# Optimization experiments

Hardware: AMD Instinct MI355X
Metric: run time of the kernel (lower is better)

## Reference

```python
import jax, jax.numpy as jnp
import numpy as np

B_SZ, T, H, N, L = 4, 512, 256, 64, 4
EPS = 1e-5

def _hippo(n):
    i = np.arange(n)[:, None]; j = np.arange(n)[None, :]
    A = np.where(i >= j, ((-1.0) ** (i - j)) * np.sqrt((2 * i + 1.0) * (2 * j + 1.0)), 0.0)
    # scale to be contractive so the 512-step dense recurrence stays finite
    A = A / (1.1 * np.linalg.norm(A, 2))
    return A.astype(np.float32)

def _xavier(key, shape):
    fan_in, fan_out = shape[1], shape[0]
    a = float(np.sqrt(6.0 / (fan_in + fan_out)))
    return jax.random.uniform(key, shape, jnp.float32, -a, a)

def setup_inputs() -> dict:
    key = jax.random.key(0)
    ks = jax.random.split(key, 8)
    x = jax.random.normal(ks[0], (B_SZ, T, H), jnp.float32)
    A = jnp.broadcast_to(jnp.asarray(_hippo(N)), (L, N, N))
    Bm = jnp.stack([_xavier(jax.random.fold_in(ks[1], l), (N, H)) for l in range(L)])
    Cm = jnp.stack([_xavier(jax.random.fold_in(ks[2], l), (H, N)) for l in range(L)])
    Dm = jnp.stack([_xavier(jax.random.fold_in(ks[3], l), (H, H)) for l in range(L)])
    Win = _xavier(ks[4], (H, H)); bin_ = jnp.zeros((H,), jnp.float32)
    Wout = _xavier(ks[5], (H, H)); bout = jnp.zeros((H,), jnp.float32)
    return {"x": x, "Win": Win, "bin_": bin_, "Wout": Wout, "bout": bout,
            "A": A, "Bm": Bm, "Cm": Cm, "Dm": Dm}

def _ln(x):
    m = jnp.mean(x, -1, keepdims=True)
    v = jnp.mean((x - m) ** 2, -1, keepdims=True)
    return (x - m) / jnp.sqrt(v + EPS)

def _ssm_layer(h, A, B, C, D):
    # h: (B,T,H); dense state (B,N,H)
    Cbar = C.mean(0)            # mean over output rows (matches C_state.mean(dim=2))
    BT = B.T                    # (H,N)
    DT = D.T                    # (H,H)
    def step(state, u):        # state (B,N,H), u (B,H)
        y = jnp.einsum('bnh,n->bh', state, Cbar) + u @ DT   # output uses pre-update state
        new_state = jnp.einsum('nm,bmh->bnh', A, state) + (u @ BT)[:, :, None]
        return new_state, y
    state0 = jnp.zeros((h.shape[0], A.shape[0], h.shape[2]), h.dtype)
    _, ys = jax.lax.scan(step, state0, jnp.swapaxes(h, 0, 1))  # scan over T
    y = jnp.swapaxes(ys, 0, 1)
    y = jax.nn.gelu(y, approximate=False) + h   # GELU -> (dropout=0) -> residual
    return _ln(y)

def reference(x, Win, bin_, Wout, bout, A, Bm, Cm, Dm):
    h = x @ Win.T + bin_
    for l in range(L):
        h = _ssm_layer(h, A[l], Bm[l], Cm[l], Dm[l])
    h = _ln(h)
    return h @ Wout.T + bout
```

## Files before the change

### kernel.cpp

```cpp
#include <hip/hip_runtime.h>

#define TSEQ 512
#define HDIM 256
#define NDIM 64
#define LC   48
#define YSTR 260
#define NWB  128

typedef __attribute__((ext_vector_type(4))) float  f32x4;
typedef __attribute__((ext_vector_type(8))) short  s16x8;
typedef __attribute__((ext_vector_type(4))) unsigned short u16x4;
typedef unsigned long long u64;
typedef unsigned short us;

#define MFMA16 __builtin_amdgcn_mfma_f32_16x16x32_bf16

__device__ __forceinline__ float wave_red(float v) {
#pragma unroll
    for (int m = 1; m < 64; m <<= 1) v += __shfl_xor(v, m, 64);
    return v;
}
__device__ __forceinline__ float lane_bcast(float v, int l) {
    return __int_as_float(__builtin_amdgcn_readlane(__float_as_int(v), l));
}
__device__ __forceinline__ us f2bf(float f) {
    unsigned u = __float_as_uint(f);
    u += 0x7fffu + ((u >> 16) & 1u);
    return (us)(u >> 16);
}
__device__ __forceinline__ float bf2f(us h) {
    return __uint_as_float(((unsigned)h) << 16);
}
__device__ __forceinline__ int swz(int row, int chunk) {
    return row * 512 + (((chunk) ^ (row & 7)) << 4);
}

__device__ __forceinline__ void st_mall(float* p, float v) {
    __hip_atomic_store(p, v, __ATOMIC_RELAXED, __HIP_MEMORY_SCOPE_AGENT);
}
__device__ __forceinline__ u64 ld_mall8(const u64* p) {
    return __hip_atomic_load(p, __ATOMIC_RELAXED, __HIP_MEMORY_SCOPE_AGENT);
}
__device__ __forceinline__ void flag_set(unsigned* f) {
    __hip_atomic_store(f, 1u, __ATOMIC_RELAXED, __HIP_MEMORY_SCOPE_AGENT);
}
__device__ __forceinline__ void flag_wait(const unsigned* f) {
    while (__hip_atomic_load(f, __ATOMIC_RELAXED, __HIP_MEMORY_SCOPE_AGENT) == 0u)
        __builtin_amdgcn_s_sleep(1);
}

__global__ void __launch_bounds__(256) k_prep(
    const float* __restrict__ Win, const float* __restrict__ Wout,
    const float* __restrict__ Bm, const float* __restrict__ Dm,
    const float* __restrict__ Cm, const float* __restrict__ A,
    us* __restrict__ Win_bf, us* __restrict__ Wout_bf,
    us* __restrict__ Bm_bf, us* __restrict__ Dm_bf,
    float* __restrict__ cbar_g, float* __restrict__ wA8,
    unsigned* __restrict__ flags)
{
    __shared__ __align__(16) float Pa[4096];
    __shared__ __align__(16) float Pb[4096];
    const int gid = blockIdx.x, tid = threadIdx.x;

    if (gid < 128) {
        for (int q = gid * 256 + tid; q < 114688; q += 32768) {
            const float* s; us* d; int off;
            if (q < 16384)      { s = Win;  d = Win_bf;  off = q; }
            else if (q < 32768) { s = Wout; d = Wout_bf; off = q - 16384; }
            else if (q < 49152) { s = Bm;   d = Bm_bf;   off = q - 32768; }
            else                { s = Dm;   d = Dm_bf;   off = q - 49152; }
            f32x4 v = ((const f32x4*)s)[off];
            u16x4 p; p[0] = f2bf(v[0]); p[1] = f2bf(v[1]); p[2] = f2bf(v[2]); p[3] = f2bf(v[3]);
            ((u16x4*)d)[off] = p;
        }
        return;
    }
    if (gid == 128) {
        for (int i = tid; i < 4 + 4 * NWB; i += 256)
            __hip_atomic_store(&flags[i], 0u, __ATOMIC_RELAXED, __HIP_MEMORY_SCOPE_AGENT);
        const int l = tid >> 6, n = tid & 63;
        const float* cp = Cm + (size_t)l * HDIM * NDIM + n;
        float s0 = 0.f, s1 = 0.f, s2 = 0.f, s3 = 0.f;
        for (int h = 0; h < HDIM; h += 4) {
            s0 += cp[(h + 0) * NDIM]; s1 += cp[(h + 1) * NDIM];
            s2 += cp[(h + 2) * NDIM]; s3 += cp[(h + 3) * NDIM];
        }
        cbar_g[tid] = ((s0 + s1) + (s2 + s3)) * (1.0f / HDIM);
        return;
    }
    for (int q = tid; q < 1024; q += 256) ((f32x4*)Pa)[q] = ((const f32x4*)A)[q];
    __syncthreads();
    const int r0 = (tid >> 3) * 2, c0 = (tid & 7) * 8;
    const f32x4 z4 = {0.f, 0.f, 0.f, 0.f};
#pragma unroll 1
    for (int it = 0; it < 3; ++it) {
        const float* S = (it & 1) ? Pb : Pa;
        float*       D = (it & 1) ? Pa : Pb;
        f32x4 s00 = z4, s01 = z4, s10 = z4, s11 = z4;
        for (int k = 0; k < 64; ++k) {
            float a0 = S[r0 * 64 + k], a1 = S[(r0 + 1) * 64 + k];
            f32x4 b0 = *(const f32x4*)(S + k * 64 + c0);
            f32x4 b1 = *(const f32x4*)(S + k * 64 + c0 + 4);
            s00 += a0 * b0; s01 += a0 * b1; s10 += a1 * b0; s11 += a1 * b1;
        }
        *(f32x4*)(D + r0 * 64 + c0) = s00;       *(f32x4*)(D + r0 * 64 + c0 + 4) = s01;
        *(f32x4*)(D + (r0 + 1) * 64 + c0) = s10; *(f32x4*)(D + (r0 + 1) * 64 + c0 + 4) = s11;
        __syncthreads();
    }
    for (int q = tid; q < 1024; q += 256) ((f32x4*)wA8)[q] = ((const f32x4*)Pb)[q];
}

__global__ void __launch_bounds__(512, 2) k_fused(
    const float* __restrict__ x, const float* __restrict__ bin,
    const float* __restrict__ bout, const float* __restrict__ A,
    const float* __restrict__ wA8, const float* __restrict__ cbar_g,
    const us* __restrict__ Win_bf, const us* __restrict__ Wout_bf,
    const us* __restrict__ Bm_bf, const us* __restrict__ Dm_bf,
    float* __restrict__ wbuf, float* __restrict__ BiA, float* __restrict__ BiB,
    unsigned* __restrict__ flags, float* __restrict__ out)
{
    __shared__ __align__(16) char smem[53568];
    us*    xl   = (us*)smem;
    float* yl   = (float*)(smem + 8192);
    float* bwin = (float*)(smem + 24832);
    float* wlds = (float*)(smem + 41216);
    float* cfin = (float*)(smem + 53504);

    const int gid = blockIdx.x, tid = threadIdx.x;
    const int lane = tid & 63, wv = tid >> 6;
    const int m = lane & 15, cgq = lane >> 4;
    const f32x4 z4 = {0.f, 0.f, 0.f, 0.f};

    if (gid == NWB) {
        float* As  = (float*)smem;
        float* A8s = (float*)(smem + 16384);
        float* uls = (float*)(smem + 32768);
        for (int q = tid; q < 1024; q += 512) {
            ((f32x4*)As)[q]  = ((const f32x4*)A)[q];
            ((f32x4*)A8s)[q] = ((const f32x4*)wA8)[q];
        }
        __syncthreads();
        if (wv < 4) {
            const int l = wv;
            float u = cbar_g[l * 64 + lane];
            uls[(l * 8 + 0) * 64 + lane] = u;
#pragma unroll 1
            for (int s = 1; s < 8; ++s) {
                float p0 = 0.f, p1 = 0.f, p2 = 0.f, p3 = 0.f;
#pragma unroll
                for (int k = 0; k < 64; k += 4) {
                    p0 += As[(k + 0) * 64 + lane] * lane_bcast(u, k + 0);
                    p1 += As[(k + 1) * 64 + lane] * lane_bcast(u, k + 1);
                    p2 += As[(k + 2) * 64 + lane] * lane_bcast(u, k + 2);
                    p3 += As[(k + 3) * 64 + lane] * lane_bcast(u, k + 3);
                }
                u = (p0 + p1) + (p2 + p3);
                uls[(l * 8 + s) * 64 + lane] = u;
            }
        }
        __syncthreads();
        {
            const int p = wv;
            float u0 = uls[(0 * 8 + p) * 64 + lane];
            float u1 = uls[(1 * 8 + p) * 64 + lane];
            float u2 = uls[(2 * 8 + p) * 64 + lane];
            float u3 = uls[(3 * 8 + p) * 64 + lane];
#pragma unroll 1
            for (int k6 = 0; k6 < 6; ++k6) {
                const int j = p + 8 * k6;
                st_mall(&wbuf[(0 * LC + j) * 64 + lane], u0);
                st_mall(&wbuf[(1 * LC + j) * 64 + lane], u1);
                st_mall(&wbuf[(2 * LC + j) * 64 + lane], u2);
                st_mall(&wbuf[(3 * LC + j) * 64 + lane], u3);
                if (k6 < 5) {
                    float n0 = 0.f, n1 = 0.f, n2 = 0.f, n3 = 0.f;
#pragma unroll
                    for (int k = 0; k < 64; ++k) {
                        float a = A8s[k * 64 + lane];
                        n0 += a * lane_bcast(u0, k); n1 += a * lane_bcast(u1, k);
                        n2 += a * lane_bcast(u2, k); n3 += a * lane_bcast(u3, k);
                    }
                    u0 = n0; u1 = n1; u2 = n2; u3 = n3;
                }
            }
        }
        __syncthreads();
        if (tid < 4) flag_set(&flags[tid]);
        return;
    }

    const int b = gid >> 5, tb = gid & 31, t0 = tb * 16;
    const size_t grow = (size_t)(b * TSEQ + t0);

    {
        const f32x4* gs = (const f32x4*)(x + grow * HDIM);
#pragma unroll
        for (int k = 0; k < 2; ++k) {
            int q = tid + k * 512;
            int row = q >> 6, c4 = q & 63;
            f32x4 v = gs[q];
            u16x4 pk; pk[0] = f2bf(v[0]); pk[1] = f2bf(v[1]); pk[2] = f2bf(v[2]); pk[3] = f2bf(v[3]);
            *(u16x4*)((char*)xl + swz(row, c4 >> 1) + (c4 & 1) * 8) = pk;
        }
    }
    __syncthreads();

    {
        f32x4 accA = z4, accB = z4;
        const us* W0 = Win_bf + (size_t)(wv * 32 + m) * HDIM;
        const us* W1 = Win_bf + (size_t)(wv * 32 + 16 + m) * HDIM;
#pragma unroll
        for (int ks = 0; ks < 8; ++ks) {
            s16x8 av = *(const s16x8*)((const char*)xl + swz(m, ks * 4 + cgq));
            s16x8 b0 = *(const s16x8*)(W0 + ks * 32 + cgq * 8);
            s16x8 b1 = *(const s16x8*)(W1 + ks * 32 + cgq * 8);
            accA = MFMA16(av, b0, accA, 0, 0, 0);
            accB = MFMA16(av, b1, accB, 0, 0, 0);
        }
        __syncthreads();
        const int h0c = wv * 32 + m, h1c = wv * 32 + 16 + m;
        float bi0 = bin[h0c], bi1 = bin[h1c];
#pragma unroll
        for (int reg = 0; reg < 4; ++reg) {
            int trow = cgq * 4 + reg;
            *(us*)((char*)xl + swz(trow, h0c >> 3) + (h0c & 7) * 2) = f2bf(accA[reg] + bi0);
            *(us*)((char*)xl + swz(trow, h1c >> 3) + (h1c & 7) * 2) = f2bf(accB[reg] + bi1);
        }
    }
    __syncthreads();

    if (wv < 4) {
        f32x4 accb = z4;
        const us* B0 = Bm_bf + (size_t)(wv * 16 + m) * HDIM;
#pragma unroll
        for (int ks = 0; ks < 8; ++ks) {
            s16x8 av = *(const s16x8*)((const char*)xl + swz(m, ks * 4 + cgq));
            s16x8 bv = *(const s16x8*)(B0 + ks * 32 + cgq * 8);
            accb = MFMA16(av, bv, accb, 0, 0, 0);
        }
#pragma unroll
        for (int reg = 0; reg < 4; ++reg)
            st_mall(&BiA[(grow + cgq * 4 + reg) * NDIM + wv * 16 + m], accb[reg]);
    }
    __syncthreads();
    if (tid == 0) flag_set(&flags[4 + 0 * NWB + gid]);

#pragma unroll 1
    for (int l = 0; l < 4; ++l) {
        const us* Dl = Dm_bf + (size_t)l * HDIM * HDIM;
        const float* bi = (l & 1) ? BiB : BiA;
        float*       bo = (l & 1) ? BiA : BiB;

        f32x4 accA = z4, accB = z4;
        {
            const us* D0 = Dl + (size_t)(wv * 32 + m) * HDIM;
            const us* D1 = Dl + (size_t)(wv * 32 + 16 + m) * HDIM;
#pragma unroll
            for (int ks = 0; ks < 8; ++ks) {
                s16x8 av = *(const s16x8*)((const char*)xl + swz(m, ks * 4 + cgq));
                s16x8 b0 = *(const s16x8*)(D0 + ks * 32 + cgq * 8);
                s16x8 b1 = *(const s16x8*)(D1 + ks * 32 + cgq * 8);
                accA = MFMA16(av, b0, accA, 0, 0, 0);
                accB = MFMA16(av, b1, accB, 0, 0, 0);
            }
        }

        {
            const unsigned* fp = nullptr;
            if (lane == 3) fp = &flags[l];
            else if (lane < 3 && (tb - 1 - (int)lane) >= 0) fp = &flags[4 + l * NWB + gid - 1 - lane];
            if (fp) flag_wait(fp);
        }

        {
            const u64* ws8 = (const u64*)(wbuf + (size_t)l * LC * NDIM);
            for (int q = tid; q < LC * NDIM / 2; q += 512)
                ((u64*)wlds)[q] = ld_mall8(&ws8[q]);
            const u64* bi8 = (const u64*)(bi + (size_t)b * TSEQ * NDIM);
#pragma unroll
            for (int k = 0; k < 4; ++k) {
                int q = tid + k * 512;
                int r = q >> 5, cc = q & 31;
                int t = t0 - LC + r;
                ((u64*)bwin)[q] = (t >= 0) ? ld_mall8(&bi8[(size_t)t * 32 + cc]) : 0ull;
            }
        }
        __syncthreads();

        {
            const int r0 = wv * 2;
            float c0 = 0.f, c1 = 0.f;
            float v0 = bwin[(LC - 1 + r0) * NDIM + lane];
            float v1 = bwin[(LC + r0) * NDIM + lane];
#pragma unroll
            for (int j = 0; j < LC; ++j) {
                float wj = wlds[j * NDIM + lane];
                c0 += wj * v0; c1 += wj * v1;
                v1 = v0;
                int nr = LC - 2 + r0 - j; nr = nr < 0 ? 0 : nr;
                v0 = bwin[nr * NDIM + lane];
            }
            c0 = wave_red(c0); c1 = wave_red(c1);
            if (lane == 0) { cfin[r0] = c0; cfin[r0 + 1] = c1; }
        }
        __syncthreads();

#pragma unroll
        for (int nt = 0; nt < 2; ++nt) {
            int hcol = wv * 32 + nt * 16 + m;
#pragma unroll
            for (int reg = 0; reg < 4; ++reg) {
                int trow = cgq * 4 + reg;
                float val = (nt ? accB[reg] : accA[reg]) + cfin[trow];
                float g = 0.5f * val * (1.0f + erff(val * 0.70710678118654752f));
                float r = bf2f(*(const us*)((const char*)xl + swz(trow, hcol >> 3) + (hcol & 7) * 2));
                yl[trow * YSTR + hcol] = g + r;
            }
        }
        __syncthreads();

        {
            const bool last = (l == 3);
#pragma unroll
            for (int q = 0; q < 2; ++q) {
                int r = wv * 2 + q;
                f32x4 yv = *(const f32x4*)(yl + r * YSTR + lane * 4);
                float s = (yv[0] + yv[1]) + (yv[2] + yv[3]);
                float sq = yv[0] * yv[0] + yv[1] * yv[1] + yv[2] * yv[2] + yv[3] * yv[3];
                s = wave_red(s); sq = wave_red(sq);
                float mn = s * (1.0f / HDIM);
                float var = sq * (1.0f / HDIM) - mn * mn;
                float rs = rsqrtf(var + 1e-5f);
                if (last) { float vz = var * rs * rs; rs = rs * rsqrtf(vz + 1e-5f); }
                u16x4 zp;
                zp[0] = f2bf((yv[0] - mn) * rs); zp[1] = f2bf((yv[1] - mn) * rs);
                zp[2] = f2bf((yv[2] - mn) * rs); zp[3] = f2bf((yv[3] - mn) * rs);
                *(u16x4*)((char*)xl + swz(r, lane >> 1) + (lane & 1) * 8) = zp;
            }
        }
        __syncthreads();

        if (l < 3) {
            if (wv < 4) {
                f32x4 accb = z4;
                const us* B0 = Bm_bf + (size_t)(l + 1) * NDIM * HDIM + (size_t)(wv * 16 + m) * HDIM;
#pragma unroll
                for (int ks = 0; ks < 8; ++ks) {
                    s16x8 av = *(const s16x8*)((const char*)xl + swz(m, ks * 4 + cgq));
                    s16x8 bv = *(const s16x8*)(B0 + ks * 32 + cgq * 8);
                    accb = MFMA16(av, bv, accb, 0, 0, 0);
                }
#pragma unroll
                for (int reg = 0; reg < 4; ++reg)
                    st_mall(&bo[(grow + cgq * 4 + reg) * NDIM + wv * 16 + m], accb[reg]);
            }
            __syncthreads();
            if (tid == 0) flag_set(&flags[4 + (l + 1) * NWB + gid]);
        } else {
            f32x4 a2A = z4, a2B = z4;
            const us* W0 = Wout_bf + (size_t)(wv * 32 + m) * HDIM;
            const us* W1 = Wout_bf + (size_t)(wv * 32 + 16 + m) * HDIM;
#pragma unroll
            for (int ks = 0; ks < 8; ++ks) {
                s16x8 av = *(const s16x8*)((const char*)xl + swz(m, ks * 4 + cgq));
                s16x8 b0 = *(const s16x8*)(W0 + ks * 32 + cgq * 8);
                s16x8 b1 = *(const s16x8*)(W1 + ks * 32 + cgq * 8);
                a2A = MFMA16(av, b0, a2A, 0, 0, 0);
                a2B = MFMA16(av, b1, a2B, 0, 0, 0);
            }
#pragma unroll
            for (int nt = 0; nt < 2; ++nt) {
                int hcol = wv * 32 + nt * 16 + m;
                float bo2 = bout[hcol];
#pragma unroll
                for (int reg = 0; reg < 4; ++reg) {
                    int trow = cgq * 4 + reg;
                    out[(grow + trow) * HDIM + hcol] = (nt ? a2B[reg] : a2A[reg]) + bo2;
                }
            }
        }
    }
}

extern "C" void kernel_launch(void* const* d_in, const int* in_sizes, int n_in,
                              void* d_out, int out_size, void* d_ws, size_t ws_size,
                              hipStream_t stream) {
    (void)in_sizes; (void)n_in; (void)out_size; (void)ws_size;
    const float* x    = (const float*)d_in[0];
    const float* Win  = (const float*)d_in[1];
    const float* bin  = (const float*)d_in[2];
    const float* Wout = (const float*)d_in[3];
    const float* bout = (const float*)d_in[4];
    const float* A    = (const float*)d_in[5];
    const float* Bm   = (const float*)d_in[6];
    const float* Cm   = (const float*)d_in[7];
    const float* Dm   = (const float*)d_in[8];

    float* ws     = (float*)d_ws;
    float* wbuf   = ws;
    float* cbar_g = ws + 16384;
    float* wA8    = ws + 17408;
    float* biA    = ws + 21504;
    float* biB    = ws + 152576;
    unsigned* flags = (unsigned*)(ws + 283648);
    us* Win_bf  = (us*)(ws + 284672);
    us* Wout_bf = Win_bf + 65536;
    us* Bm_bf   = Wout_bf + 65536;
    us* Dm_bf   = Bm_bf + 65536;
    float* out  = (float*)d_out;

    k_prep<<<130, 256, 0, stream>>>(Win, Wout, Bm, Dm, Cm, A,
                                    Win_bf, Wout_bf, Bm_bf, Dm_bf, cbar_g, wA8, flags);
    k_fused<<<NWB + 1, 512, 0, stream>>>(x, bin, bout, A, wA8, cbar_g,
                                         Win_bf, Wout_bf, Bm_bf, Dm_bf,
                                         wbuf, biA, biB, flags, out);
}
```

Before: 71.94 us.

## Merge prep into fused kernel, use 256 blocks of 8 rows with dedicated chunk-scan waves

Removes the separate prep kernel. Weights are now converted fp32→bf16 inline when loaded for each MFMA, and cbar and A^8 are computed inside a designated block that also does its own row work. The grid doubles to 256 blocks of 8 timesteps each, with 768 threads per block: 8 waves handle the matmuls and 4 extra waves handle flag waiting and the chunked state convolution, synchronised through an LDS counter. The aim is to cut the kernel launch and weight-conversion pass and to overlap the D matmul with the cross-block dependency wait. The cost is that half the MFMA rows are wasted (16-row tiles for 8 rows), fp32 weights are reloaded and repacked in every block, and the scan chain has more links.

```diff
diff --git a/kernel.cpp b/kernel.cpp
--- a/kernel.cpp
+++ b/kernel.cpp
@@ -4,8 +4,10 @@
 #define HDIM 256
 #define NDIM 64
 #define LC   48
+#define MT   8
 #define YSTR 260
-#define NWB  128
+#define NWRK 256
+#define WGID 255
 
 typedef __attribute__((ext_vector_type(4))) float  f32x4;
 typedef __attribute__((ext_vector_type(8))) short  s16x8;
@@ -34,7 +36,14 @@
 __device__ __forceinline__ int swz(int row, int chunk) {
     return row * 512 + (((chunk) ^ (row & 7)) << 4);
 }
-
+__device__ __forceinline__ s16x8 pack8(f32x4 a, f32x4 b) {
+    s16x8 r;
+    r[0] = (short)f2bf(a[0]); r[1] = (short)f2bf(a[1]);
+    r[2] = (short)f2bf(a[2]); r[3] = (short)f2bf(a[3]);
+    r[4] = (short)f2bf(b[0]); r[5] = (short)f2bf(b[1]);
+    r[6] = (short)f2bf(b[2]); r[7] = (short)f2bf(b[3]);
+    return r;
+}
 __device__ __forceinline__ void st_mall(float* p, float v) {
     __hip_atomic_store(p, v, __ATOMIC_RELAXED, __HIP_MEMORY_SCOPE_AGENT);
 }
@@ -49,101 +58,62 @@
         __builtin_amdgcn_s_sleep(1);
 }
 
-__global__ void __launch_bounds__(256) k_prep(
-    const float* __restrict__ Win, const float* __restrict__ Wout,
-    const float* __restrict__ Bm, const float* __restrict__ Dm,
-    const float* __restrict__ Cm, const float* __restrict__ A,
-    us* __restrict__ Win_bf, us* __restrict__ Wout_bf,
-    us* __restrict__ Bm_bf, us* __restrict__ Dm_bf,
-    float* __restrict__ cbar_g, float* __restrict__ wA8,
-    unsigned* __restrict__ flags)
-{
-    __shared__ __align__(16) float Pa[4096];
-    __shared__ __align__(16) float Pb[4096];
-    const int gid = blockIdx.x, tid = threadIdx.x;
-
-    if (gid < 128) {
-        for (int q = gid * 256 + tid; q < 114688; q += 32768) {
-            const float* s; us* d; int off;
-            if (q < 16384)      { s = Win;  d = Win_bf;  off = q; }
-            else if (q < 32768) { s = Wout; d = Wout_bf; off = q - 16384; }
-            else if (q < 49152) { s = Bm;   d = Bm_bf;   off = q - 32768; }
-            else                { s = Dm;   d = Dm_bf;   off = q - 49152; }
-            f32x4 v = ((const f32x4*)s)[off];
-            u16x4 p; p[0] = f2bf(v[0]); p[1] = f2bf(v[1]); p[2] = f2bf(v[2]); p[3] = f2bf(v[3]);
-            ((u16x4*)d)[off] = p;
-        }
-        return;
-    }
-    if (gid == 128) {
-        for (int i = tid; i < 4 + 4 * NWB; i += 256)
-            __hip_atomic_store(&flags[i], 0u, __ATOMIC_RELAXED, __HIP_MEMORY_SCOPE_AGENT);
-        const int l = tid >> 6, n = tid & 63;
-        const float* cp = Cm + (size_t)l * HDIM * NDIM + n;
-        float s0 = 0.f, s1 = 0.f, s2 = 0.f, s3 = 0.f;
-        for (int h = 0; h < HDIM; h += 4) {
-            s0 += cp[(h + 0) * NDIM]; s1 += cp[(h + 1) * NDIM];
-            s2 += cp[(h + 2) * NDIM]; s3 += cp[(h + 3) * NDIM];
-        }
-        cbar_g[tid] = ((s0 + s1) + (s2 + s3)) * (1.0f / HDIM);
-        return;
-    }
-    for (int q = tid; q < 1024; q += 256) ((f32x4*)Pa)[q] = ((const f32x4*)A)[q];
-    __syncthreads();
-    const int r0 = (tid >> 3) * 2, c0 = (tid & 7) * 8;
-    const f32x4 z4 = {0.f, 0.f, 0.f, 0.f};
-#pragma unroll 1
-    for (int it = 0; it < 3; ++it) {
-        const float* S = (it & 1) ? Pb : Pa;
-        float*       D = (it & 1) ? Pa : Pb;
-        f32x4 s00 = z4, s01 = z4, s10 = z4, s11 = z4;
-        for (int k = 0; k < 64; ++k) {
-            float a0 = S[r0 * 64 + k], a1 = S[(r0 + 1) * 64 + k];
-            f32x4 b0 = *(const f32x4*)(S + k * 64 + c0);
-            f32x4 b1 = *(const f32x4*)(S + k * 64 + c0 + 4);
-            s00 += a0 * b0; s01 += a0 * b1; s10 += a1 * b0; s11 += a1 * b1;
-        }
-        *(f32x4*)(D + r0 * 64 + c0) = s00;       *(f32x4*)(D + r0 * 64 + c0 + 4) = s01;
-        *(f32x4*)(D + (r0 + 1) * 64 + c0) = s10; *(f32x4*)(D + (r0 + 1) * 64 + c0 + 4) = s11;
-        __syncthreads();
-    }
-    for (int q = tid; q < 1024; q += 256) ((f32x4*)wA8)[q] = ((const f32x4*)Pb)[q];
-}
-
-__global__ void __launch_bounds__(512, 2) k_fused(
+__global__ void __launch_bounds__(768, 1) k_fused(
     const float* __restrict__ x, const float* __restrict__ bin,
     const float* __restrict__ bout, const float* __restrict__ A,
-    const float* __restrict__ wA8, const float* __restrict__ cbar_g,
-    const us* __restrict__ Win_bf, const us* __restrict__ Wout_bf,
-    const us* __restrict__ Bm_bf, const us* __restrict__ Dm_bf,
+    const float* __restrict__ Bm, const float* __restrict__ Cm,
+    const float* __restrict__ Dm, const float* __restrict__ Win,
+    const float* __restrict__ Wout,
     float* __restrict__ wbuf, float* __restrict__ BiA, float* __restrict__ BiB,
     unsigned* __restrict__ flags, float* __restrict__ out)
 {
-    __shared__ __align__(16) char smem[53568];
+    __shared__ __align__(16) char smem[49216];
     us*    xl   = (us*)smem;
     float* yl   = (float*)(smem + 8192);
-    float* bwin = (float*)(smem + 24832);
-    float* wlds = (float*)(smem + 41216);
-    float* cfin = (float*)(smem + 53504);
+    float* bwin = (float*)(smem + 16512);
+    float* wlds = (float*)(smem + 30848);
+    float* cfin = (float*)(smem + 43136);
+    unsigned* cnt = (unsigned*)(smem + 43168);
+    float* As  = (float*)(smem + 8192);
+    float* A8s = (float*)(smem + 24576);
+    float* uls = (float*)(smem + 40960);
 
     const int gid = blockIdx.x, tid = threadIdx.x;
     const int lane = tid & 63, wv = tid >> 6;
     const int m = lane & 15, cgq = lane >> 4;
     const f32x4 z4 = {0.f, 0.f, 0.f, 0.f};
-
-    if (gid == NWB) {
-        float* As  = (float*)smem;
-        float* A8s = (float*)(smem + 16384);
-        float* uls = (float*)(smem + 32768);
-        for (int q = tid; q < 1024; q += 512) {
-            ((f32x4*)As)[q]  = ((const f32x4*)A)[q];
-            ((f32x4*)A8s)[q] = ((const f32x4*)wA8)[q];
-        }
-        __syncthreads();
+    const int b = gid >> 6, tb = gid & 63, t0 = tb * MT;
+    const size_t grow = (size_t)(b * TSEQ + t0);
+
+    if (gid == WGID) {
+        float cbv = 0.f;
         if (wv < 4) {
-            const int l = wv;
-            float u = cbar_g[l * 64 + lane];
-            uls[(l * 8 + 0) * 64 + lane] = u;
+            const float* cp = Cm + (size_t)wv * HDIM * NDIM + lane;
+            float s0 = 0.f, s1 = 0.f, s2 = 0.f, s3 = 0.f;
+            for (int h = 0; h < HDIM; h += 4) {
+                s0 += cp[(h + 0) * NDIM]; s1 += cp[(h + 1) * NDIM];
+                s2 += cp[(h + 2) * NDIM]; s3 += cp[(h + 3) * NDIM];
+            }
+            cbv = ((s0 + s1) + (s2 + s3)) * (1.0f / HDIM);
+        } else if (wv < 8) {
+            int t = tid - 256;
+            for (int q = t; q < 1024; q += 256) ((f32x4*)As)[q] = ((const f32x4*)A)[q];
+        } else {
+            int t = tid - 512;
+            const f32x4* gs = (const f32x4*)(x + grow * HDIM);
+#pragma unroll
+            for (int k = 0; k < 2; ++k) {
+                int q = t + k * 256;
+                int row = q >> 6, c4 = q & 63;
+                f32x4 v = gs[q];
+                u16x4 pk; pk[0] = f2bf(v[0]); pk[1] = f2bf(v[1]); pk[2] = f2bf(v[2]); pk[3] = f2bf(v[3]);
+                *(u16x4*)((char*)xl + swz(row, c4 >> 1) + (c4 & 1) * 8) = pk;
+            }
+        }
+        __syncthreads();
+        if (wv < 4) {
+            float u = cbv;
+            uls[(wv * 8 + 0) * 64 + lane] = u;
 #pragma unroll 1
             for (int s = 1; s < 8; ++s) {
                 float p0 = 0.f, p1 = 0.f, p2 = 0.f, p3 = 0.f;
@@ -155,227 +125,284 @@
                     p3 += As[(k + 3) * 64 + lane] * lane_bcast(u, k + 3);
                 }
                 u = (p0 + p1) + (p2 + p3);
-                uls[(l * 8 + s) * 64 + lane] = u;
-            }
-        }
-        __syncthreads();
-        {
-            const int p = wv;
-            float u0 = uls[(0 * 8 + p) * 64 + lane];
-            float u1 = uls[(1 * 8 + p) * 64 + lane];
-            float u2 = uls[(2 * 8 + p) * 64 + lane];
-            float u3 = uls[(3 * 8 + p) * 64 + lane];
+                uls[(wv * 8 + s) * 64 + lane] = u;
+            }
+        } else if (wv < 8) {
+            int t = tid - 256;
+            int r = t >> 2, c0 = (t & 3) * 16;
+            f32x4 a0 = z4, a1 = z4, a2 = z4, a3 = z4;
+            for (int k = 0; k < 64; ++k) {
+                float av = As[r * 64 + k];
+                const f32x4* bp = (const f32x4*)(As + k * 64 + c0);
+                a0 += av * bp[0]; a1 += av * bp[1]; a2 += av * bp[2]; a3 += av * bp[3];
+            }
+            f32x4* dp = (f32x4*)(A8s + r * 64 + c0);
+            dp[0] = a0; dp[1] = a1; dp[2] = a2; dp[3] = a3;
+        }
+        __syncthreads();
+        if (wv < 8) {
+            int r = tid >> 3, c0 = (tid & 7) * 8;
+            f32x4 a0 = z4, a1 = z4;
+            for (int k = 0; k < 64; ++k) {
+                float av = A8s[r * 64 + k];
+                const f32x4* bp = (const f32x4*)(A8s + k * 64 + c0);
+                a0 += av * bp[0]; a1 += av * bp[1];
+            }
+            __syncthreads();
+            *(f32x4*)(As + r * 64 + c0) = a0;
+            *(f32x4*)(As + r * 64 + c0 + 4) = a1;
+        } else __syncthreads();
+        __syncthreads();
+        if (wv < 8) {
+            int r = tid >> 3, c0 = (tid & 7) * 8;
+            f32x4 a0 = z4, a1 = z4;
+            for (int k = 0; k < 64; ++k) {
+                float av = As[r * 64 + k];
+                const f32x4* bp = (const f32x4*)(As + k * 64 + c0);
+                a0 += av * bp[0]; a1 += av * bp[1];
+            }
+            __syncthreads();
+            *(f32x4*)(A8s + r * 64 + c0) = a0;
+            *(f32x4*)(A8s + r * 64 + c0 + 4) = a1;
+        } else { __syncthreads(); }
+        __syncthreads();
+        if (wv < 8) {
+            float u = uls[wv * 64 + lane];
 #pragma unroll 1
             for (int k6 = 0; k6 < 6; ++k6) {
-                const int j = p + 8 * k6;
-                st_mall(&wbuf[(0 * LC + j) * 64 + lane], u0);
-                st_mall(&wbuf[(1 * LC + j) * 64 + lane], u1);
-                st_mall(&wbuf[(2 * LC + j) * 64 + lane], u2);
-                st_mall(&wbuf[(3 * LC + j) * 64 + lane], u3);
+                st_mall(&wbuf[(size_t)(wv + 8 * k6) * 64 + lane], u);
                 if (k6 < 5) {
-                    float n0 = 0.f, n1 = 0.f, n2 = 0.f, n3 = 0.f;
+                    float n0 = 0.f;
+#pragma unroll
+                    for (int k = 0; k < 64; ++k)
+                        n0 += A8s[k * 64 + lane] * lane_bcast(u, k);
+                    u = n0;
+                }
+            }
+        }
+        __syncthreads();
+        if (tid == 0) flag_set(&flags[0]);
+        if (wv < 8) {
+            float u1 = uls[(8 + wv) * 64 + lane];
+            float u2 = uls[(16 + wv) * 64 + lane];
+            float u3 = uls[(24 + wv) * 64 + lane];
+#pragma unroll 1
+            for (int k6 = 0; k6 < 6; ++k6) {
+                const int j = wv + 8 * k6;
+                st_mall(&wbuf[(size_t)(1 * LC + j) * 64 + lane], u1);
+                st_mall(&wbuf[(size_t)(2 * LC + j) * 64 + lane], u2);
+                st_mall(&wbuf[(size_t)(3 * LC + j) * 64 + lane], u3);
+                if (k6 < 5) {
+                    float n1 = 0.f, n2 = 0.f, n3 = 0.f;
 #pragma unroll
                     for (int k = 0; k < 64; ++k) {
                         float a = A8s[k * 64 + lane];
-                        n0 += a * lane_bcast(u0, k); n1 += a * lane_bcast(u1, k);
-                        n2 += a * lane_bcast(u2, k); n3 += a * lane_bcast(u3, k);
+                        n1 += a * lane_bcast(u1, k); n2 += a * lane_bcast(u2, k);
+                        n3 += a * lane_bcast(u3, k);
                     }
-                    u0 = n0; u1 = n1; u2 = n2; u3 = n3;
-                }
-            }
-        }
-        __syncthreads();
-        if (tid < 4) flag_set(&flags[tid]);
-        return;
-    }
-
-    const int b = gid >> 5, tb = gid & 31, t0 = tb * 16;
-    const size_t grow = (size_t)(b * TSEQ + t0);
-
-    {
-        const f32x4* gs = (const f32x4*)(x + grow * HDIM);
-#pragma unroll
-        for (int k = 0; k < 2; ++k) {
-            int q = tid + k * 512;
-            int row = q >> 6, c4 = q & 63;
-            f32x4 v = gs[q];
+                    u1 = n1; u2 = n2; u3 = n3;
+                }
+            }
+        }
+        __syncthreads();
+        if (tid < 3) flag_set(&flags[1 + tid]);
+    } else {
+        if (tid < 512) {
+            const f32x4* gs = (const f32x4*)(x + grow * HDIM);
+            int row = tid >> 6, c4 = tid & 63;
+            f32x4 v = gs[tid];
             u16x4 pk; pk[0] = f2bf(v[0]); pk[1] = f2bf(v[1]); pk[2] = f2bf(v[2]); pk[3] = f2bf(v[3]);
             *(u16x4*)((char*)xl + swz(row, c4 >> 1) + (c4 & 1) * 8) = pk;
         }
     }
+    if (tid < 4) cnt[tid] = 0u;
     __syncthreads();
 
-    {
-        f32x4 accA = z4, accB = z4;
-        const us* W0 = Win_bf + (size_t)(wv * 32 + m) * HDIM;
-        const us* W1 = Win_bf + (size_t)(wv * 32 + 16 + m) * HDIM;
+    f32x4 accA = z4, accB = z4;
+    if (wv < 8) {
+        const float* W0 = Win + (size_t)(wv * 32 + m) * HDIM;
+        const float* W1 = W0 + (size_t)16 * HDIM;
 #pragma unroll
         for (int ks = 0; ks < 8; ++ks) {
             s16x8 av = *(const s16x8*)((const char*)xl + swz(m, ks * 4 + cgq));
-            s16x8 b0 = *(const s16x8*)(W0 + ks * 32 + cgq * 8);
-            s16x8 b1 = *(const s16x8*)(W1 + ks * 32 + cgq * 8);
-            accA = MFMA16(av, b0, accA, 0, 0, 0);
-            accB = MFMA16(av, b1, accB, 0, 0, 0);
-        }
-        __syncthreads();
-        const int h0c = wv * 32 + m, h1c = wv * 32 + 16 + m;
+            const float* p0 = W0 + ks * 32 + cgq * 8;
+            const float* p1 = W1 + ks * 32 + cgq * 8;
+            accA = MFMA16(av, pack8(*(const f32x4*)p0, *(const f32x4*)(p0 + 4)), accA, 0, 0, 0);
+            accB = MFMA16(av, pack8(*(const f32x4*)p1, *(const f32x4*)(p1 + 4)), accB, 0, 0, 0);
+        }
+    }
+    __syncthreads();
+    if (wv < 8) {
+        const int h0c = wv * 32 + m, h1c = h0c + 16;
         float bi0 = bin[h0c], bi1 = bin[h1c];
 #pragma unroll
         for (int reg = 0; reg < 4; ++reg) {
             int trow = cgq * 4 + reg;
-            *(us*)((char*)xl + swz(trow, h0c >> 3) + (h0c & 7) * 2) = f2bf(accA[reg] + bi0);
-            *(us*)((char*)xl + swz(trow, h1c >> 3) + (h1c & 7) * 2) = f2bf(accB[reg] + bi1);
+            if (trow < MT) {
+                *(us*)((char*)xl + swz(trow, h0c >> 3) + (h0c & 7) * 2) = f2bf(accA[reg] + bi0);
+                *(us*)((char*)xl + swz(trow, h1c >> 3) + (h1c & 7) * 2) = f2bf(accB[reg] + bi1);
+            }
         }
     }
     __syncthreads();
-
     if (wv < 4) {
         f32x4 accb = z4;
-        const us* B0 = Bm_bf + (size_t)(wv * 16 + m) * HDIM;
+        const float* B0 = Bm + (size_t)(wv * 16 + m) * HDIM;
 #pragma unroll
         for (int ks = 0; ks < 8; ++ks) {
             s16x8 av = *(const s16x8*)((const char*)xl + swz(m, ks * 4 + cgq));
-            s16x8 bv = *(const s16x8*)(B0 + ks * 32 + cgq * 8);
-            accb = MFMA16(av, bv, accb, 0, 0, 0);
-        }
-#pragma unroll
-        for (int reg = 0; reg < 4; ++reg)
-            st_mall(&BiA[(grow + cgq * 4 + reg) * NDIM + wv * 16 + m], accb[reg]);
+            const float* p0 = B0 + ks * 32 + cgq * 8;
+            accb = MFMA16(av, pack8(*(const f32x4*)p0, *(const f32x4*)(p0 + 4)), accb, 0, 0, 0);
+        }
+#pragma unroll
+        for (int reg = 0; reg < 4; ++reg) {
+            int trow = cgq * 4 + reg;
+            if (trow < MT)
+                st_mall(&BiA[(grow + trow) * NDIM + wv * 16 + m], accb[reg]);
+        }
     }
     __syncthreads();
-    if (tid == 0) flag_set(&flags[4 + 0 * NWB + gid]);
+    if (tid == 0) flag_set(&flags[4 + 0 * NWRK + gid]);
 
 #pragma unroll 1
     for (int l = 0; l < 4; ++l) {
-        const us* Dl = Dm_bf + (size_t)l * HDIM * HDIM;
         const float* bi = (l & 1) ? BiB : BiA;
         float*       bo = (l & 1) ? BiA : BiB;
 
-        f32x4 accA = z4, accB = z4;
-        {
-            const us* D0 = Dl + (size_t)(wv * 32 + m) * HDIM;
-            const us* D1 = Dl + (size_t)(wv * 32 + 16 + m) * HDIM;
+        f32x4 dA = z4, dB = z4;
+        if (wv < 8) {
+            const float* D0 = Dm + (size_t)l * HDIM * HDIM + (size_t)(wv * 32 + m) * HDIM;
+            const float* D1 = D0 + (size_t)16 * HDIM;
 #pragma unroll
             for (int ks = 0; ks < 8; ++ks) {
                 s16x8 av = *(const s16x8*)((const char*)xl + swz(m, ks * 4 + cgq));
-                s16x8 b0 = *(const s16x8*)(D0 + ks * 32 + cgq * 8);
-                s16x8 b1 = *(const s16x8*)(D1 + ks * 32 + cgq * 8);
-                accA = MFMA16(av, b0, accA, 0, 0, 0);
-                accB = MFMA16(av, b1, accB, 0, 0, 0);
-            }
-        }
-
-        {
-            const unsigned* fp = nullptr;
-            if (lane == 3) fp = &flags[l];
-            else if (lane < 3 && (tb - 1 - (int)lane) >= 0) fp = &flags[4 + l * NWB + gid - 1 - lane];
-            if (fp) flag_wait(fp);
-        }
-
-        {
-            const u64* ws8 = (const u64*)(wbuf + (size_t)l * LC * NDIM);
-            for (int q = tid; q < LC * NDIM / 2; q += 512)
-                ((u64*)wlds)[q] = ld_mall8(&ws8[q]);
-            const u64* bi8 = (const u64*)(bi + (size_t)b * TSEQ * NDIM);
-#pragma unroll
-            for (int k = 0; k < 4; ++k) {
-                int q = tid + k * 512;
-                int r = q >> 5, cc = q & 31;
-                int t = t0 - LC + r;
-                ((u64*)bwin)[q] = (t >= 0) ? ld_mall8(&bi8[(size_t)t * 32 + cc]) : 0ull;
-            }
-        }
-        __syncthreads();
-
-        {
-            const int r0 = wv * 2;
-            float c0 = 0.f, c1 = 0.f;
-            float v0 = bwin[(LC - 1 + r0) * NDIM + lane];
-            float v1 = bwin[(LC + r0) * NDIM + lane];
-#pragma unroll
-            for (int j = 0; j < LC; ++j) {
-                float wj = wlds[j * NDIM + lane];
-                c0 += wj * v0; c1 += wj * v1;
-                v1 = v0;
-                int nr = LC - 2 + r0 - j; nr = nr < 0 ? 0 : nr;
-                v0 = bwin[nr * NDIM + lane];
-            }
-            c0 = wave_red(c0); c1 = wave_red(c1);
-            if (lane == 0) { cfin[r0] = c0; cfin[r0 + 1] = c1; }
-        }
-        __syncthreads();
-
-#pragma unroll
-        for (int nt = 0; nt < 2; ++nt) {
-            int hcol = wv * 32 + nt * 16 + m;
-#pragma unroll
-            for (int reg = 0; reg < 4; ++reg) {
-                int trow = cgq * 4 + reg;
-                float val = (nt ? accB[reg] : accA[reg]) + cfin[trow];
-                float g = 0.5f * val * (1.0f + erff(val * 0.70710678118654752f));
-                float r = bf2f(*(const us*)((const char*)xl + swz(trow, hcol >> 3) + (hcol & 7) * 2));
-                yl[trow * YSTR + hcol] = g + r;
-            }
-        }
-        __syncthreads();
-
-        {
-            const bool last = (l == 3);
-#pragma unroll
-            for (int q = 0; q < 2; ++q) {
-                int r = wv * 2 + q;
-                f32x4 yv = *(const f32x4*)(yl + r * YSTR + lane * 4);
-                float s = (yv[0] + yv[1]) + (yv[2] + yv[3]);
-                float sq = yv[0] * yv[0] + yv[1] * yv[1] + yv[2] * yv[2] + yv[3] * yv[3];
-                s = wave_red(s); sq = wave_red(sq);
-                float mn = s * (1.0f / HDIM);
-                float var = sq * (1.0f / HDIM) - mn * mn;
-                float rs = rsqrtf(var + 1e-5f);
-                if (last) { float vz = var * rs * rs; rs = rs * rsqrtf(vz + 1e-5f); }
-                u16x4 zp;
-                zp[0] = f2bf((yv[0] - mn) * rs); zp[1] = f2bf((yv[1] - mn) * rs);
-                zp[2] = f2bf((yv[2] - mn) * rs); zp[3] = f2bf((yv[3] - mn) * rs);
-                *(u16x4*)((char*)xl + swz(r, lane >> 1) + (lane & 1) * 8) = zp;
-            }
+                const float* p0 = D0 + ks * 32 + cgq * 8;
+                const float* p1 = D1 + ks * 32 + cgq * 8;
+                dA = MFMA16(av, pack8(*(const f32x4*)p0, *(const f32x4*)(p0 + 4)), dA, 0, 0, 0);
+                dB = MFMA16(av, pack8(*(const f32x4*)p1, *(const f32x4*)(p1 + 4)), dB, 0, 0, 0);
+            }
+        } else {
+            const int cw = wv - 8;
+            {
+                const unsigned* fp = nullptr;
+                if (lane == 6) fp = &flags[l];
+                else if (lane < 6 && (tb - 1 - (int)lane) >= 0)
+                    fp = &flags[4 + l * NWRK + gid - 1 - lane];
+                if (fp) flag_wait(fp);
+            }
+            {
+                const int ct = cw * 64 + lane;
+                const u64* ws8 = (const u64*)(wbuf + (size_t)l * LC * NDIM);
+#pragma unroll
+                for (int k = 0; k < 6; ++k)
+                    ((u64*)wlds)[ct + k * 256] = ld_mall8(&ws8[ct + k * 256]);
+                const u64* bi8 = (const u64*)(bi + (size_t)b * TSEQ * NDIM);
+#pragma unroll
+                for (int k = 0; k < 7; ++k) {
+                    int q = ct + k * 256;
+                    int r = q >> 5, cc = q & 31;
+                    int t = t0 - LC + r;
+                    ((u64*)bwin)[q] = (t >= 0) ? ld_mall8(&bi8[(size_t)t * 32 + cc]) : 0ull;
+                }
+            }
+            if (lane == 0)
+                __hip_atomic_fetch_add(&cnt[l], 1u, __ATOMIC_ACQ_REL, __HIP_MEMORY_SCOPE_WORKGROUP);
+            while (__hip_atomic_load(&cnt[l], __ATOMIC_ACQUIRE, __HIP_MEMORY_SCOPE_WORKGROUP) < 4u)
+                __builtin_amdgcn_s_sleep(0);
+            {
+                const int r0 = cw * 2;
+                float c0 = 0.f, c1 = 0.f;
+                float vlo = bwin[(LC - 1 + r0) * NDIM + lane];
+                float vhi = bwin[(LC + r0) * NDIM + lane];
+#pragma unroll
+                for (int j = 0; j < LC; ++j) {
+                    float wj = wlds[j * NDIM + lane];
+                    c0 += wj * vlo; c1 += wj * vhi;
+                    vhi = vlo;
+                    int nr = LC - 2 + r0 - j; nr = nr < 0 ? 0 : nr;
+                    vlo = bwin[nr * NDIM + lane];
+                }
+                c0 = wave_red(c0); c1 = wave_red(c1);
+                if (lane == 0) { cfin[r0] = c0; cfin[r0 + 1] = c1; }
+            }
+        }
+        __syncthreads();
+
+        if (wv < 8) {
+#pragma unroll
+            for (int nt = 0; nt < 2; ++nt) {
+                int hcol = wv * 32 + nt * 16 + m;
+#pragma unroll
+                for (int reg = 0; reg < 4; ++reg) {
+                    int trow = cgq * 4 + reg;
+                    if (trow < MT) {
+                        float val = (nt ? dB[reg] : dA[reg]) + cfin[trow];
+                        float g = 0.5f * val * (1.0f + erff(val * 0.70710678118654752f));
+                        float r = bf2f(*(const us*)((const char*)xl + swz(trow, hcol >> 3) + (hcol & 7) * 2));
+                        yl[trow * YSTR + hcol] = g + r;
+                    }
+                }
+            }
+        }
+        __syncthreads();
+
+        if (wv < 8) {
+            f32x4 yv = *(const f32x4*)(yl + wv * YSTR + lane * 4);
+            float s = (yv[0] + yv[1]) + (yv[2] + yv[3]);
+            float sq = yv[0] * yv[0] + yv[1] * yv[1] + yv[2] * yv[2] + yv[3] * yv[3];
+            s = wave_red(s); sq = wave_red(sq);
+            float mn = s * (1.0f / HDIM);
+            float var = sq * (1.0f / HDIM) - mn * mn;
+            float rs = rsqrtf(var + 1e-5f);
+            if (l == 3) { float vz = var * rs * rs; rs = rs * rsqrtf(vz + 1e-5f); }
+            u16x4 zp;
+            zp[0] = f2bf((yv[0] - mn) * rs); zp[1] = f2bf((yv[1] - mn) * rs);
+            zp[2] = f2bf((yv[2] - mn) * rs); zp[3] = f2bf((yv[3] - mn) * rs);
+            *(u16x4*)((char*)xl + swz(wv, lane >> 1) + (lane & 1) * 8) = zp;
         }
         __syncthreads();
 
         if (l < 3) {
             if (wv < 4) {
                 f32x4 accb = z4;
-                const us* B0 = Bm_bf + (size_t)(l + 1) * NDIM * HDIM + (size_t)(wv * 16 + m) * HDIM;
+                const float* B0 = Bm + (size_t)(l + 1) * NDIM * HDIM + (size_t)(wv * 16 + m) * HDIM;
 #pragma unroll
                 for (int ks = 0; ks < 8; ++ks) {
                     s16x8 av = *(const s16x8*)((const char*)xl + swz(m, ks * 4 + cgq));
-                    s16x8 bv = *(const s16x8*)(B0 + ks * 32 + cgq * 8);
-                    accb = MFMA16(av, bv, accb, 0, 0, 0);
-                }
-#pragma unroll
-                for (int reg = 0; reg < 4; ++reg)
-                    st_mall(&bo[(grow + cgq * 4 + reg) * NDIM + wv * 16 + m], accb[reg]);
-            }
-            __syncthreads();
-            if (tid == 0) flag_set(&flags[4 + (l + 1) * NWB + gid]);
-        } else {
-            f32x4 a2A = z4, a2B = z4;
-            const us* W0 = Wout_bf + (size_t)(wv * 32 + m) * HDIM;
-            const us* W1 = Wout_bf + (size_t)(wv * 32 + 16 + m) * HDIM;
-#pragma unroll
-            for (int ks = 0; ks < 8; ++ks) {
-                s16x8 av = *(const s16x8*)((const char*)xl + swz(m, ks * 4 + cgq));
-                s16x8 b0 = *(const s16x8*)(W0 + ks * 32 + cgq * 8);
-                s16x8 b1 = *(const s16x8*)(W1 + ks * 32 + cgq * 8);
-                a2A = MFMA16(av, b0, a2A, 0, 0, 0);
-                a2B = MFMA16(av, b1, a2B, 0, 0, 0);
-            }
-#pragma unroll
-            for (int nt = 0; nt < 2; ++nt) {
-                int hcol = wv * 32 + nt * 16 + m;
-                float bo2 = bout[hcol];
+                    const float* p0 = B0 + ks * 32 + cgq * 8;
+                    accb = MFMA16(av, pack8(*(const f32x4*)p0, *(const f32x4*)(p0 + 4)), accb, 0, 0, 0);
+                }
 #pragma unroll
                 for (int reg = 0; reg < 4; ++reg) {
                     int trow = cgq * 4 + reg;
-                    out[(grow + trow) * HDIM + hcol] = (nt ? a2B[reg] : a2A[reg]) + bo2;
+                    if (trow < MT)
+                        st_mall(&bo[(grow + trow) * NDIM + wv * 16 + m], accb[reg]);
+                }
+            }
+            __syncthreads();
+            if (tid == 0) flag_set(&flags[4 + (l + 1) * NWRK + gid]);
+        } else {
+            f32x4 oA = z4, oB = z4;
+            if (wv < 8) {
+                const float* W0 = Wout + (size_t)(wv * 32 + m) * HDIM;
+                const float* W1 = W0 + (size_t)16 * HDIM;
+#pragma unroll
+                for (int ks = 0; ks < 8; ++ks) {
+                    s16x8 av = *(const s16x8*)((const char*)xl + swz(m, ks * 4 + cgq));
+                    const float* p0 = W0 + ks * 32 + cgq * 8;
+                    const float* p1 = W1 + ks * 32 + cgq * 8;
+                    oA = MFMA16(av, pack8(*(const f32x4*)p0, *(const f32x4*)(p0 + 4)), oA, 0, 0, 0);
+                    oB = MFMA16(av, pack8(*(const f32x4*)p1, *(const f32x4*)(p1 + 4)), oB, 0, 0, 0);
+                }
+                const int h0c = wv * 32 + m, h1c = h0c + 16;
+                float bo0 = bout[h0c], bo1 = bout[h1c];
+#pragma unroll
+                for (int reg = 0; reg < 4; ++reg) {
+                    int trow = cgq * 4 + reg;
+                    if (trow < MT) {
+                        out[(grow + trow) * HDIM + h0c] = oA[reg] + bo0;
+                        out[(grow + trow) * HDIM + h1c] = oB[reg] + bo1;
+                    }
                 }
             }
         }
@@ -396,22 +423,14 @@
     const float* Cm   = (const float*)d_in[7];
     const float* Dm   = (const float*)d_in[8];
 
-    float* ws     = (float*)d_ws;
-    float* wbuf   = ws;
-    float* cbar_g = ws + 16384;
-    float* wA8    = ws + 17408;
-    float* biA    = ws + 21504;
-    float* biB    = ws + 152576;
-    unsigned* flags = (unsigned*)(ws + 283648);
-    us* Win_bf  = (us*)(ws + 284672);
-    us* Wout_bf = Win_bf + 65536;
-    us* Bm_bf   = Wout_bf + 65536;
-    us* Dm_bf   = Bm_bf + 65536;
-    float* out  = (float*)d_out;
-
-    k_prep<<<130, 256, 0, stream>>>(Win, Wout, Bm, Dm, Cm, A,
-                                    Win_bf, Wout_bf, Bm_bf, Dm_bf, cbar_g, wA8, flags);
-    k_fused<<<NWB + 1, 512, 0, stream>>>(x, bin, bout, A, wA8, cbar_g,
-                                         Win_bf, Wout_bf, Bm_bf, Dm_bf,
-                                         wbuf, biA, biB, flags, out);
-}
+    float* ws   = (float*)d_ws;
+    float* wbuf = ws;
+    float* BiA  = ws + 16384;
+    float* BiB  = ws + 147456;
+    unsigned* flags = (unsigned*)(ws + 278528);
+    float* out = (float*)d_out;
+
+    hipMemsetAsync(flags, 0, (4 + 4 * NWRK) * sizeof(unsigned), stream);
+    k_fused<<<NWRK, 768, 0, stream>>>(x, bin, bout, A, Bm, Cm, Dm, Win, Wout,
+                                      wbuf, BiA, BiB, flags, out);
+}
```

Result: slower. 99.65 us (+38.5%).
